# Kernel optimization log

Hardware: AMD Instinct MI355X
Metric: run time of the kernel (lower is better)

Reference implementation:

```python
import jax, jax.numpy as jnp
import numpy as np

N = 10000
E = 160000
D_IN = 512
D_OUT = 512


def setup_inputs() -> dict:
    key = jax.random.key(0)
    k1, k2, k3, k4, k5 = jax.random.split(key, 5)
    x = jax.random.normal(k1, (N, D_IN), dtype=jnp.float32)
    edge_index = jax.random.randint(k2, (2, E), 0, N, dtype=jnp.int64)
    edge_attr = jax.random.uniform(k3, (E,), dtype=jnp.float32)
    W = jax.random.normal(k4, (D_IN, D_OUT), dtype=jnp.float32) * 0.05
    b = jax.random.normal(k5, (D_OUT,), dtype=jnp.float32) * 0.05
    return {"x": x, "edge_index": edge_index, "edge_attr": edge_attr, "W": W, "b": b}


def reference(x, edge_index, edge_attr, W, b):
    # PyG GCNConv with normalize=True, add_self_loops=True, edge_weight=edge_attr.
    n = x.shape[0]
    row, col = edge_index[0], edge_index[1]
    # Add self loops with weight 1.0 (fill_value=1.)
    loop = jnp.arange(n, dtype=edge_index.dtype)
    row_f = jnp.concatenate([row, loop])      # [E+N] source nodes
    col_f = jnp.concatenate([col, loop])      # [E+N] target nodes
    ew = jnp.concatenate([edge_attr, jnp.ones((n,), dtype=edge_attr.dtype)])
    # Symmetric normalization: deg computed over target index (col)
    deg = jax.ops.segment_sum(ew, col_f, num_segments=n)
    dinv = jnp.where(deg > 0, jax.lax.rsqrt(deg), 0.0)
    norm = dinv[row_f] * ew * dinv[col_f]     # [E+N]
    # Linear transform (no bias inside lin), then gather-scale-scatter
    h = x @ W                                  # [N, D_OUT]
    msg = h[row_f] * norm[:, None]             # [E+N, D_OUT]
    out = jax.ops.segment_sum(msg, col_f, num_segments=n)
    return out + b
```

## Files before the change

kernel.cpp:

```cpp
#include <hip/hip_runtime.h>

#define NN 10000
#define EE 160000
#define DD 512
#define CAP 128

typedef float floatx4 __attribute__((ext_vector_type(4)));
typedef short short8 __attribute__((ext_vector_type(8)));

#define AS3(p) ((__attribute__((address_space(3))) void*)(p))
#define AS1(p) ((const __attribute__((address_space(1))) void*)(p))

static __device__ __forceinline__ unsigned short f2bf(float f) {
    unsigned int u = __float_as_uint(f);
    unsigned int r = (u + 0x7fffu + ((u >> 16) & 1u)) >> 16;
    return (unsigned short)r;
}
static __device__ __forceinline__ float bflo(unsigned int u) {
    return __uint_as_float(u << 16);
}
static __device__ __forceinline__ float bfhi(unsigned int u) {
    return __uint_as_float(u & 0xffff0000u);
}


#define XB_BLOCKS 5000
#define WT_BLOCKS 256
#define EDGE_BLOCKS 625

__global__ __launch_bounds__(256) void k_prep(const float* __restrict__ x,
                                              const float* __restrict__ W,
                                              const int* __restrict__ row,
                                              const int* __restrict__ col,
                                              const float* __restrict__ ew,
                                              unsigned short* __restrict__ xb,
                                              unsigned short* __restrict__ wtb,
                                              float* __restrict__ deg,
                                              int* __restrict__ cursor,
                                              uint2* __restrict__ erw) {
    const int b = blockIdx.x;
    const int tid = threadIdx.x;
    if (b < XB_BLOCKS) {
        int gid = b * 256 + tid;
        float4 v = *(const float4*)&x[(size_t)gid * 4];
        unsigned int p0 = (unsigned int)f2bf(v.x) | ((unsigned int)f2bf(v.y) << 16);
        unsigned int p1 = (unsigned int)f2bf(v.z) | ((unsigned int)f2bf(v.w) << 16);
        *(uint2*)&xb[(size_t)gid * 4] = make_uint2(p0, p1);
    } else if (b < XB_BLOCKS + WT_BLOCKS) {
        __shared__ float T[32][33];
        int idx = b - XB_BLOCKS;
        int bi = idx & 15;
        int bj = idx >> 4;
        int r0 = tid >> 5;
        int cc = tid & 31;
        #pragma unroll
        for (int k = 0; k < 4; k++) {
            int r = r0 + k * 8;
            T[r][cc] = W[(size_t)(bi * 32 + r) * DD + bj * 32 + cc];
        }
        __syncthreads();
        #pragma unroll
        for (int k = 0; k < 4; k++) {
            int r = r0 + k * 8;
            wtb[(size_t)(bj * 32 + r) * DD + bi * 32 + cc] = f2bf(T[cc][r]);
        }
    } else {
        int e = (b - XB_BLOCKS - WT_BLOCKS) * 256 + tid;
        int r = row[e];
        int t = col[e];
        float w = ew[e];
        atomicAdd(&deg[t], w);
        int p = atomicAdd(&cursor[t], 1);
        if (p < CAP) erw[t * CAP + p] = make_uint2((unsigned int)r, __float_as_uint(w));
    }
}


__global__ __launch_bounds__(256) void k_gemm_mfma(const unsigned short* __restrict__ xb,
                                                   const unsigned short* __restrict__ wtb,
                                                   const float* __restrict__ deg,
                                                   unsigned short* __restrict__ hb) {
    __shared__ unsigned short As[64 * 32];
    __shared__ unsigned short Bs[128 * 32];

    const int tid = threadIdx.x;
    const int wave = tid >> 6;
    const int lane = tid & 63;

    const int bm = blockIdx.x * 64;
    const int bn = blockIdx.y * 128;

    const int wm = (wave >> 1) * 32;
    const int wn = (wave & 1) * 64;

    const int fm = lane & 15;
    const int kb = (lane >> 4) * 8;

    floatx4 acc[2][4];
    #pragma unroll
    for (int i = 0; i < 2; i++)
        #pragma unroll
        for (int j = 0; j < 4; j++)
            acc[i][j] = (floatx4){0.f, 0.f, 0.f, 0.f};

    const int srow = lane >> 2;
    const int scol = (lane & 3) * 8;

    for (int k0 = 0; k0 < DD; k0 += 32) {
        {
            int r = wave * 16 + srow;
            int gr = bm + r; if (gr > NN - 1) gr = NN - 1;
            __builtin_amdgcn_global_load_lds(AS1(xb + (size_t)gr * DD + k0 + scol),
                                             AS3(&As[wave * 512]), 16, 0, 0);
        }
        #pragma unroll
        for (int cc = 0; cc < 2; cc++) {
            int c = wave + cc * 4;
            int nr = bn + c * 16 + srow;
            __builtin_amdgcn_global_load_lds(AS1(wtb + (size_t)nr * DD + k0 + scol),
                                             AS3(&Bs[c * 512]), 16, 0, 0);
        }
        __syncthreads();

        short8 af[2], bfr[4];
        #pragma unroll
        for (int mi = 0; mi < 2; mi++)
            af[mi] = *(const short8*)&As[(wm + mi * 16 + fm) * 32 + kb];
        #pragma unroll
        for (int ni = 0; ni < 4; ni++)
            bfr[ni] = *(const short8*)&Bs[(wn + ni * 16 + fm) * 32 + kb];

        #pragma unroll
        for (int mi = 0; mi < 2; mi++)
            #pragma unroll
            for (int ni = 0; ni < 4; ni++)
                acc[mi][ni] = __builtin_amdgcn_mfma_f32_16x16x32_bf16(af[mi], bfr[ni], acc[mi][ni], 0, 0, 0);

        __syncthreads();
    }

    float dv[2][4];
    #pragma unroll
    for (int mi = 0; mi < 2; mi++) {
        int rbase = bm + wm + mi * 16 + (lane >> 4) * 4;
        #pragma unroll
        for (int j = 0; j < 4; j++) {
            int rg = rbase + j; if (rg > NN - 1) rg = NN - 1;
            dv[mi][j] = rsqrtf(deg[rg] + 1.0f);
        }
    }

    #pragma unroll
    for (int mi = 0; mi < 2; mi++) {
        #pragma unroll
        for (int ni = 0; ni < 4; ni++) {
            int colg = bn + wn + ni * 16 + (lane & 15);
            int rbase = bm + wm + mi * 16 + (lane >> 4) * 4;
            #pragma unroll
            for (int j = 0; j < 4; j++) {
                int rg = rbase + j;
                if (rg < NN) hb[(size_t)rg * DD + colg] = f2bf(acc[mi][ni][j] * dv[mi][j]);
            }
        }
    }
}


#define EDGE_FMA1(P, W) \
    acc0 += bflo(P) * W; acc1 += bfhi(P) * W;

__global__ __launch_bounds__(256, 8) void k_aggregate(const int* __restrict__ cursor,
                                                      const uint2* __restrict__ erw,
                                                      const unsigned short* __restrict__ hb,
                                                      const float* __restrict__ deg,
                                                      const float* __restrict__ bias,
                                                      float* __restrict__ out) {
    const int w = threadIdx.x >> 6;
    const int t = threadIdx.x & 63;
    const int bid = blockIdx.x;
    const int quarter = bid & 3;
    const int i = (bid >> 2) * 4 + w;
    const int c = quarter * 128 + t * 2;

    __shared__ int   s_r[4][CAP];
    __shared__ float s_w[4][CAP];

    int cnt = cursor[i];
    if (cnt > CAP) cnt = CAP;
    const uint2* bkt = erw + (size_t)i * CAP;
    if (t < cnt)      { uint2 p = bkt[t];      s_r[w][t]      = (int)p.x; s_w[w][t]      = __uint_as_float(p.y); }
    if (t + 64 < cnt) { uint2 p = bkt[t + 64]; s_r[w][t + 64] = (int)p.x; s_w[w][t + 64] = __uint_as_float(p.y); }

    float dv = rsqrtf(deg[i] + 1.0f);
    unsigned int hv = *(const unsigned int*)&hb[(size_t)i * DD + c];
    float2 bv = *(const float2*)&bias[c];

    __syncthreads();

    float acc0 = 0.f, acc1 = 0.f;

    int j = 0;
    for (; j + 8 <= cnt; j += 8) {
        unsigned int p0 = *(const unsigned int*)&hb[(size_t)s_r[w][j    ] * DD + c];
        unsigned int p1 = *(const unsigned int*)&hb[(size_t)s_r[w][j + 1] * DD + c];
        unsigned int p2 = *(const unsigned int*)&hb[(size_t)s_r[w][j + 2] * DD + c];
        unsigned int p3 = *(const unsigned int*)&hb[(size_t)s_r[w][j + 3] * DD + c];
        unsigned int p4 = *(const unsigned int*)&hb[(size_t)s_r[w][j + 4] * DD + c];
        unsigned int p5 = *(const unsigned int*)&hb[(size_t)s_r[w][j + 5] * DD + c];
        unsigned int p6 = *(const unsigned int*)&hb[(size_t)s_r[w][j + 6] * DD + c];
        unsigned int p7 = *(const unsigned int*)&hb[(size_t)s_r[w][j + 7] * DD + c];
        float w0 = s_w[w][j],     w1 = s_w[w][j + 1], w2 = s_w[w][j + 2], w3 = s_w[w][j + 3];
        float w4 = s_w[w][j + 4], w5 = s_w[w][j + 5], w6 = s_w[w][j + 6], w7 = s_w[w][j + 7];
        EDGE_FMA1(p0, w0) EDGE_FMA1(p1, w1) EDGE_FMA1(p2, w2) EDGE_FMA1(p3, w3)
        EDGE_FMA1(p4, w4) EDGE_FMA1(p5, w5) EDGE_FMA1(p6, w6) EDGE_FMA1(p7, w7)
    }
    for (; j + 4 <= cnt; j += 4) {
        unsigned int p0 = *(const unsigned int*)&hb[(size_t)s_r[w][j    ] * DD + c];
        unsigned int p1 = *(const unsigned int*)&hb[(size_t)s_r[w][j + 1] * DD + c];
        unsigned int p2 = *(const unsigned int*)&hb[(size_t)s_r[w][j + 2] * DD + c];
        unsigned int p3 = *(const unsigned int*)&hb[(size_t)s_r[w][j + 3] * DD + c];
        float w0 = s_w[w][j], w1 = s_w[w][j + 1], w2 = s_w[w][j + 2], w3 = s_w[w][j + 3];
        EDGE_FMA1(p0, w0) EDGE_FMA1(p1, w1) EDGE_FMA1(p2, w2) EDGE_FMA1(p3, w3)
    }
    for (; j < cnt; j++) {
        unsigned int p0 = *(const unsigned int*)&hb[(size_t)s_r[w][j] * DD + c];
        float w0 = s_w[w][j];
        EDGE_FMA1(p0, w0)
    }

    float2 o;
    o.x = (acc0 + bflo(hv)) * dv + bv.x;
    o.y = (acc1 + bfhi(hv)) * dv + bv.y;
    *(float2*)&out[(size_t)i * DD + c] = o;
}

extern "C" void kernel_launch(void* const* d_in, const int* in_sizes, int n_in,
                              void* d_out, int out_size, void* d_ws, size_t ws_size,
                              hipStream_t stream) {
    const float* x  = (const float*)d_in[0];
    const int*   ei = (const int*)d_in[1];
    const float* ea = (const float*)d_in[2];
    const float* W  = (const float*)d_in[3];
    const float* b  = (const float*)d_in[4];
    float* out = (float*)d_out;

    char* ws = (char*)d_ws;
    unsigned short* hb   = (unsigned short*)ws;
    unsigned short* xb   = (unsigned short*)(ws + 10240000);
    unsigned short* wtb  = (unsigned short*)(ws + 20480000);
    float* deg    = (float*)(ws + 21004288);
    int*   cursor = (int*)  (ws + 21045248);
    uint2* erw    = (uint2*)(ws + 21086208);

    const int* row = ei;
    const int* col = ei + EE;

    hipMemsetAsync(deg, 0, 81920, stream);

    k_prep<<<XB_BLOCKS + WT_BLOCKS + EDGE_BLOCKS, 256, 0, stream>>>(x, W, row, col, ea,
                                                                    xb, wtb, deg, cursor, erw);

    dim3 ggrid((NN + 63) / 64, DD / 128);
    k_gemm_mfma<<<ggrid, 256, 0, stream>>>(xb, wtb, deg, hb);

    k_aggregate<<<NN, 256, 0, stream>>>(cursor, erw, hb, deg, b, out);
}
```

Measured before the change: 133.1 us.

## Fuse x-to-bf16 conversion into GEMM and retile to full-width 32-row blocks

The separate pass that converts x to bf16 in prep is removed. The GEMM now reads fp32 x directly, converts it in registers and stores it to LDS. The GEMM tile changes to 32 rows by the full 512 columns, so each x row is read only once, with each wave owning 128 columns and holding 16 accumulators. This drops a 20MB write and read round trip, but the A load is now synchronous register staging rather than an async LDS load. Each block also reloads all of W^T per k-step, and there are fewer blocks (313), which raises register pressure.

Result: slower. 137.4 us (+3.3%).

```diff
diff --git a/kernel.cpp b/kernel.cpp
--- a/kernel.cpp
+++ b/kernel.cpp
@@ -16,6 +16,9 @@
     unsigned int r = (u + 0x7fffu + ((u >> 16) & 1u)) >> 16;
     return (unsigned short)r;
 }
+static __device__ __forceinline__ unsigned int pack2bf(float a, float b) {
+    return (unsigned int)f2bf(a) | ((unsigned int)f2bf(b) << 16);
+}
 static __device__ __forceinline__ float bflo(unsigned int u) {
     return __uint_as_float(u << 16);
 }
@@ -24,33 +27,23 @@
 }
 
 
-#define XB_BLOCKS 5000
 #define WT_BLOCKS 256
 #define EDGE_BLOCKS 625
 
-__global__ __launch_bounds__(256) void k_prep(const float* __restrict__ x,
-                                              const float* __restrict__ W,
+__global__ __launch_bounds__(256) void k_prep(const float* __restrict__ W,
                                               const int* __restrict__ row,
                                               const int* __restrict__ col,
                                               const float* __restrict__ ew,
-                                              unsigned short* __restrict__ xb,
                                               unsigned short* __restrict__ wtb,
                                               float* __restrict__ deg,
                                               int* __restrict__ cursor,
                                               uint2* __restrict__ erw) {
     const int b = blockIdx.x;
     const int tid = threadIdx.x;
-    if (b < XB_BLOCKS) {
-        int gid = b * 256 + tid;
-        float4 v = *(const float4*)&x[(size_t)gid * 4];
-        unsigned int p0 = (unsigned int)f2bf(v.x) | ((unsigned int)f2bf(v.y) << 16);
-        unsigned int p1 = (unsigned int)f2bf(v.z) | ((unsigned int)f2bf(v.w) << 16);
-        *(uint2*)&xb[(size_t)gid * 4] = make_uint2(p0, p1);
-    } else if (b < XB_BLOCKS + WT_BLOCKS) {
+    if (b < WT_BLOCKS) {
         __shared__ float T[32][33];
-        int idx = b - XB_BLOCKS;
-        int bi = idx & 15;
-        int bj = idx >> 4;
+        int bi = b & 15;
+        int bj = b >> 4;
         int r0 = tid >> 5;
         int cc = tid & 31;
         #pragma unroll
@@ -65,7 +58,7 @@
             wtb[(size_t)(bj * 32 + r) * DD + bi * 32 + cc] = f2bf(T[cc][r]);
         }
     } else {
-        int e = (b - XB_BLOCKS - WT_BLOCKS) * 256 + tid;
+        int e = (b - WT_BLOCKS) * 256 + tid;
         int r = row[e];
         int t = col[e];
         float w = ew[e];
@@ -76,64 +69,63 @@
 }
 
 
-__global__ __launch_bounds__(256) void k_gemm_mfma(const unsigned short* __restrict__ xb,
+__global__ __launch_bounds__(256) void k_gemm_mfma(const float* __restrict__ x,
                                                    const unsigned short* __restrict__ wtb,
                                                    const float* __restrict__ deg,
                                                    unsigned short* __restrict__ hb) {
-    __shared__ unsigned short As[64 * 32];
-    __shared__ unsigned short Bs[128 * 32];
+    __shared__ unsigned short As[32 * 32];
+    __shared__ unsigned short Bs[512 * 32];
 
     const int tid = threadIdx.x;
     const int wave = tid >> 6;
     const int lane = tid & 63;
 
-    const int bm = blockIdx.x * 64;
-    const int bn = blockIdx.y * 128;
-
-    const int wm = (wave >> 1) * 32;
-    const int wn = (wave & 1) * 64;
+    const int bm = blockIdx.x * 32;
+    const int wn = wave * 128;
 
     const int fm = lane & 15;
     const int kb = (lane >> 4) * 8;
 
-    floatx4 acc[2][4];
+    floatx4 acc[2][8];
     #pragma unroll
     for (int i = 0; i < 2; i++)
         #pragma unroll
-        for (int j = 0; j < 4; j++)
+        for (int j = 0; j < 8; j++)
             acc[i][j] = (floatx4){0.f, 0.f, 0.f, 0.f};
+
+    const int ar = tid >> 3;
+    const int acg = (tid & 7) * 4;
+    int agr = bm + ar; if (agr > NN - 1) agr = NN - 1;
+    const float* asrc = x + (size_t)agr * DD + acg;
 
     const int srow = lane >> 2;
     const int scol = (lane & 3) * 8;
 
     for (int k0 = 0; k0 < DD; k0 += 32) {
+        #pragma unroll
+        for (int cc = 0; cc < 8; cc++) {
+            int nr = wave * 128 + cc * 16 + srow;
+            __builtin_amdgcn_global_load_lds(AS1(wtb + (size_t)nr * DD + k0 + scol),
+                                             AS3(&Bs[(wave * 128 + cc * 16) * 32]), 16, 0, 0);
+        }
         {
-            int r = wave * 16 + srow;
-            int gr = bm + r; if (gr > NN - 1) gr = NN - 1;
-            __builtin_amdgcn_global_load_lds(AS1(xb + (size_t)gr * DD + k0 + scol),
-                                             AS3(&As[wave * 512]), 16, 0, 0);
-        }
-        #pragma unroll
-        for (int cc = 0; cc < 2; cc++) {
-            int c = wave + cc * 4;
-            int nr = bn + c * 16 + srow;
-            __builtin_amdgcn_global_load_lds(AS1(wtb + (size_t)nr * DD + k0 + scol),
-                                             AS3(&Bs[c * 512]), 16, 0, 0);
+            float4 v = *(const float4*)(asrc + k0);
+            *(uint2*)&As[ar * 32 + acg] = make_uint2(pack2bf(v.x, v.y), pack2bf(v.z, v.w));
         }
         __syncthreads();
 
-        short8 af[2], bfr[4];
+        short8 af[2], bfr[8];
         #pragma unroll
         for (int mi = 0; mi < 2; mi++)
-            af[mi] = *(const short8*)&As[(wm + mi * 16 + fm) * 32 + kb];
-        #pragma unroll
-        for (int ni = 0; ni < 4; ni++)
+            af[mi] = *(const short8*)&As[(mi * 16 + fm) * 32 + kb];
+        #pragma unroll
+        for (int ni = 0; ni < 8; ni++)
             bfr[ni] = *(const short8*)&Bs[(wn + ni * 16 + fm) * 32 + kb];
 
         #pragma unroll
         for (int mi = 0; mi < 2; mi++)
             #pragma unroll
-            for (int ni = 0; ni < 4; ni++)
+            for (int ni = 0; ni < 8; ni++)
                 acc[mi][ni] = __builtin_amdgcn_mfma_f32_16x16x32_bf16(af[mi], bfr[ni], acc[mi][ni], 0, 0, 0);
 
         __syncthreads();
@@ -142,7 +134,7 @@
     float dv[2][4];
     #pragma unroll
     for (int mi = 0; mi < 2; mi++) {
-        int rbase = bm + wm + mi * 16 + (lane >> 4) * 4;
+        int rbase = bm + mi * 16 + (lane >> 4) * 4;
         #pragma unroll
         for (int j = 0; j < 4; j++) {
             int rg = rbase + j; if (rg > NN - 1) rg = NN - 1;
@@ -153,9 +145,9 @@
     #pragma unroll
     for (int mi = 0; mi < 2; mi++) {
         #pragma unroll
-        for (int ni = 0; ni < 4; ni++) {
-            int colg = bn + wn + ni * 16 + (lane & 15);
-            int rbase = bm + wm + mi * 16 + (lane >> 4) * 4;
+        for (int ni = 0; ni < 8; ni++) {
+            int colg = wn + ni * 16 + (lane & 15);
+            int rbase = bm + mi * 16 + (lane >> 4) * 4;
             #pragma unroll
             for (int j = 0; j < 4; j++) {
                 int rg = rbase + j;
@@ -246,22 +238,19 @@
 
     char* ws = (char*)d_ws;
     unsigned short* hb   = (unsigned short*)ws;
-    unsigned short* xb   = (unsigned short*)(ws + 10240000);
-    unsigned short* wtb  = (unsigned short*)(ws + 20480000);
-    float* deg    = (float*)(ws + 21004288);
-    int*   cursor = (int*)  (ws + 21045248);
-    uint2* erw    = (uint2*)(ws + 21086208);
+    unsigned short* wtb  = (unsigned short*)(ws + 10240000);
+    float* deg    = (float*)(ws + 10764288);
+    int*   cursor = (int*)  (ws + 10805248);
+    uint2* erw    = (uint2*)(ws + 10846208);
 
     const int* row = ei;
     const int* col = ei + EE;
 
     hipMemsetAsync(deg, 0, 81920, stream);
 
-    k_prep<<<XB_BLOCKS + WT_BLOCKS + EDGE_BLOCKS, 256, 0, stream>>>(x, W, row, col, ea,
-                                                                    xb, wtb, deg, cursor, erw);
-
-    dim3 ggrid((NN + 63) / 64, DD / 128);
-    k_gemm_mfma<<<ggrid, 256, 0, stream>>>(xb, wtb, deg, hb);
+    k_prep<<<WT_BLOCKS + EDGE_BLOCKS, 256, 0, stream>>>(W, row, col, ea, wtb, deg, cursor, erw);
+
+    k_gemm_mfma<<<(NN + 31) / 32, 256, 0, stream>>>(x, wtb, deg, hb);
 
     k_aggregate<<<NN, 256, 0, stream>>>(cursor, erw, hb, deg, b, out);
 }
```
